# Kernel tuning notes

Hardware: AMD Instinct MI355X
Metric: run time of the kernel (lower is better)

Reference implementation:

```python
import jax, jax.numpy as jnp
import numpy as np
import math

B, S, D_MODEL = 4, 2048, 1024
H, D_HEAD = 16, 64
INIT_RANGE = 0.02


def setup_inputs() -> dict:
    key = jax.random.key(0)
    ks = jax.random.split(key, 10)
    x = jax.random.normal(ks[0], (B, S, D_MODEL), dtype=jnp.float32)
    # torch Linear(in,out): y = x @ W.T + b. We store weights pre-transposed as [H, in, out].
    u = lambda k, shape: jax.random.uniform(k, shape, dtype=jnp.float32, minval=-INIT_RANGE, maxval=INIT_RANGE)
    wq = u(ks[1], (H, D_MODEL, D_HEAD))
    wk = u(ks[2], (H, D_MODEL, D_HEAD))
    wv = u(ks[3], (H, D_MODEL, D_HEAD))
    wo = u(ks[4], (H, D_HEAD, D_MODEL))
    # biases: torch default init is uniform(-1/sqrt(fan_in), 1/sqrt(fan_in)); values don't matter for correctness harness
    bq = u(ks[5], (H, D_HEAD))
    bk = u(ks[6], (H, D_HEAD))
    bv = u(ks[7], (H, D_HEAD))
    bo = u(ks[8], (H, D_MODEL))
    return {"normalized_resid_pre": x, "wq": wq, "bq": bq, "wk": wk, "bk": bk,
            "wv": wv, "bv": bv, "wo": wo, "bo": bo}


def reference(normalized_resid_pre, wq, bq, wk, bk, wv, bv, wo, bo):
    x = normalized_resid_pre  # [B, S, D]
    # Batched multi-head QKV projections (original does a python loop per head)
    q = jnp.einsum('bsd,hde->bhse', x, wq) + bq[None, :, None, :]  # [B,H,S,dh]
    k = jnp.einsum('bsd,hde->bhse', x, wk) + bk[None, :, None, :]
    v = jnp.einsum('bsd,hde->bhse', x, wv) + bv[None, :, None, :]
    scale = 1.0 / math.sqrt(D_HEAD)  # cfg.global_d_head, used unconditionally
    scores = jnp.einsum('bhse,bhte->bhst', q, k) * scale  # [B,H,S,S], non-causal
    attn = jax.nn.softmax(scores, axis=-1)
    heads = jnp.einsum('bhst,bhte->bhse', attn, v)  # [B,H,S,dh]
    # per-head output projections, summed over heads (= sum of per-head Linear outputs)
    out = jnp.einsum('bhse,hed->bsd', heads, wo) + jnp.sum(bo, axis=0)[None, None, :]
    return out
```

## Files before the change

### kernel.cpp

```cpp
#include <hip/hip_runtime.h>
#include <hip/hip_bf16.h>
#include <math.h>


typedef __attribute__((ext_vector_type(8))) short bf16x8;
typedef __attribute__((ext_vector_type(4))) float f32x4;

#define GLDS16(gsrc, lbase) \
    __builtin_amdgcn_global_load_lds((const __attribute__((address_space(1))) void*)(gsrc), \
                                     (__attribute__((address_space(3))) void*)(lbase), 16, 0, 0)

static __device__ __forceinline__ ushort f2bf(float f) {
    __bf16 h = (__bf16)f;
    return *reinterpret_cast<ushort*>(&h);
}
static __device__ __forceinline__ unsigned pk_bf16(float a, float b) {
    return (unsigned)f2bf(a) | ((unsigned)f2bf(b) << 16);
}
static __device__ __forceinline__ float clampf(float v) {
    return fminf(fmaxf(v, -1e30f), 1e30f);
}

__global__ void cvt_x(const float* __restrict__ x, ushort* __restrict__ xb) {
    int idx = blockIdx.x * 256 + threadIdx.x;
    float4 a = ((const float4*)x)[idx * 2];
    float4 b = ((const float4*)x)[idx * 2 + 1];
    uint4 o;
    o.x = pk_bf16(a.x, a.y);
    o.y = pk_bf16(a.z, a.w);
    o.z = pk_bf16(b.x, b.y);
    o.w = pk_bf16(b.z, b.w);
    ((uint4*)xb)[idx] = o;
}

__global__ void pack_wqkv(const float* __restrict__ wq, const float* __restrict__ wk,
                          const float* __restrict__ wv, const float* __restrict__ bq,
                          const float* __restrict__ bk, const float* __restrict__ bv,
                          ushort* __restrict__ WT, float* __restrict__ biasc) {
    __shared__ __align__(16) ushort Lt[64][72];
    int bid = blockIdx.x;
    int kt = bid & 15, h = (bid >> 4) & 15, proj = bid >> 8;
    const float* w  = (proj == 0) ? wq : (proj == 1) ? wk : wv;
    const float* bb = (proj == 0) ? bq : (proj == 1) ? bk : bv;
    int t = threadIdx.x;
    int e = t & 63, kr = t >> 6;
    const float* src = w + (size_t)h * 65536 + (size_t)kt * 64 * 64 + e;
    #pragma unroll
    for (int i = 0; i < 16; ++i) {
        int kl = kr * 16 + i;
        Lt[e][kl] = f2bf(src[(size_t)kl * 64]);
    }
    if (kt == 0 && t < 64) biasc[proj * 1024 + h * 64 + t] = bb[h * 64 + t];
    __syncthreads();
    int eo = t >> 2, kc = (t & 3) * 16;
    size_t dst = (size_t)(proj * 1024 + h * 64 + eo) * 1024 + kt * 64 + kc;
    *(bf16x8*)(WT + dst)     = *(const bf16x8*)(&Lt[eo][kc]);
    *(bf16x8*)(WT + dst + 8) = *(const bf16x8*)(&Lt[eo][kc + 8]);
}
__global__ void pack_wo(const float* __restrict__ wo, const float* __restrict__ bo,
                        ushort* __restrict__ WoT, float* __restrict__ biaso) {
    __shared__ __align__(16) ushort Lt[64][72];
    int bid = blockIdx.x;
    int het = bid & 15, dt = bid >> 4;
    int t = threadIdx.x;
    int dl = t & 63, hw = t >> 6;
    #pragma unroll
    for (int i = 0; i < 16; ++i) {
        int hel = hw * 16 + i;
        Lt[dl][hel] = f2bf(wo[(size_t)(het * 64 + hel) * 1024 + dt * 64 + dl]);
    }
    if (het == 0 && t < 64) {
        int d = dt * 64 + t;
        float s = 0.f;
        for (int hh = 0; hh < 16; ++hh) s += bo[hh * 1024 + d];
        biaso[d] = s;
    }
    __syncthreads();
    int do_ = t >> 2, hc = (t & 3) * 16;
    size_t dst = (size_t)(dt * 64 + do_) * 1024 + het * 64 + hc;
    *(bf16x8*)(WoT + dst)     = *(const bf16x8*)(&Lt[do_][hc]);
    *(bf16x8*)(WoT + dst + 8) = *(const bf16x8*)(&Lt[do_][hc + 8]);
}

__global__ __launch_bounds__(256, 2) void gemm_bt(
    const ushort* __restrict__ A, const ushort* __restrict__ Bt,
    const float* __restrict__ bias, ushort* __restrict__ C, ushort* __restrict__ Vt,
    float* __restrict__ Cf, int M, int N, int K, int ldc, int n_split)
{
    __shared__ __align__(16) ushort Al[128][64];
    __shared__ __align__(16) ushort Bl[128][64];
    const int t = threadIdx.x;
    const int lane = t & 63, wave = t >> 6;
    const int wr = wave >> 1, wc = wave & 1;
    const int quad = lane >> 4, l16 = lane & 15;
    const int row0 = blockIdx.x * 128, col0 = blockIdx.y * 128;
    const int sr = t >> 3;
    const int scx = ((t & 7) ^ (sr & 7)) * 8;
    const int xk = l16 & 7;

    f32x4 acc[4][4] = {};

    for (int kt = 0; kt < K; kt += 64) {
        char* abase = (char*)Al + wave * 1024;
        char* bbase = (char*)Bl + wave * 1024;
        const ushort* ag = A  + (size_t)(row0 + sr) * K + kt + scx;
        const ushort* bg = Bt + (size_t)(col0 + sr) * K + kt + scx;
        #pragma unroll
        for (int i = 0; i < 4; ++i) {
            GLDS16(ag + (size_t)i * 32 * K, abase + i * 4096);
            GLDS16(bg + (size_t)i * 32 * K, bbase + i * 4096);
        }
        __syncthreads();
        #pragma unroll
        for (int ks = 0; ks < 2; ++ks) {
            bf16x8 a[4], b[4];
            #pragma unroll
            for (int mi = 0; mi < 4; ++mi)
                a[mi] = *(const bf16x8*)(&Al[wr * 64 + mi * 16 + l16][((ks * 4 + quad) ^ xk) * 8]);
            #pragma unroll
            for (int ni = 0; ni < 4; ++ni)
                b[ni] = *(const bf16x8*)(&Bl[wc * 64 + ni * 16 + l16][((ks * 4 + quad) ^ xk) * 8]);
            #pragma unroll
            for (int mi = 0; mi < 4; ++mi)
                #pragma unroll
                for (int ni = 0; ni < 4; ++ni)
                    acc[mi][ni] = __builtin_amdgcn_mfma_f32_16x16x32_bf16(a[mi], b[ni], acc[mi][ni], 0, 0, 0);
        }
        __syncthreads();
    }
    #pragma unroll
    for (int mi = 0; mi < 4; ++mi) {
        int rowb = row0 + wr * 64 + mi * 16 + quad * 4;
        #pragma unroll
        for (int ni = 0; ni < 4; ++ni) {
            int col = col0 + wc * 64 + ni * 16 + l16;
            float bs = bias ? bias[col] : 0.f;
            #pragma unroll
            for (int r = 0; r < 4; ++r) {
                float v = clampf(acc[mi][ni][r] + bs);
                int row = rowb + r;
                if (Cf) {
                    Cf[(size_t)row * ldc + col] = v;
                } else if (col < n_split) {
                    C[(size_t)row * ldc + col] = f2bf(v);
                } else {
                    int bb = row >> 11, s = row & 2047;
                    int pos = (s & ~63) | (((s & 15) << 2) | ((s >> 4) & 3));
                    Vt[(size_t)bb * (1024 * 2048) + (size_t)(col - n_split) * 2048 + pos] = f2bf(v);
                }
            }
        }
    }
}

__global__ __launch_bounds__(256, 2) void attn(
    const ushort* __restrict__ QK, const ushort* __restrict__ Vt, ushort* __restrict__ O)
{
    __shared__ __align__(16) ushort Kl[64][64];
    __shared__ __align__(16) ushort Vl[64][64];
    __shared__ __align__(16) ushort Pl[4][32][72];
    const int qt = blockIdx.x, b = blockIdx.y, h = blockIdx.z;
    const int t = threadIdx.x, lane = t & 63, wave = t >> 6;
    const int quad = lane >> 4, l16 = lane & 15;
    const int rowq0 = b * 2048 + qt * 128 + wave * 32;
    const int sr = t >> 3;
    const int scx = ((t & 7) ^ (sr & 7)) * 8;
    const int xk = l16 & 7;
    const float cscale = 0.125f * 1.44269504088896340736f;
    const float M0 = 14.0f;

    bf16x8 qf[2][2];
    #pragma unroll
    for (int mi = 0; mi < 2; ++mi)
        #pragma unroll
        for (int ks = 0; ks < 2; ++ks)
            qf[mi][ks] = *(const bf16x8*)(QK + (size_t)(rowq0 + mi * 16 + l16) * 2048
                                          + h * 64 + ks * 32 + quad * 8);

    f32x4 of[2][4] = {};
    float lpart[2][4] = {};

    for (int kt = 0; kt < 2048; kt += 64) {
        {
            char* kbase = (char*)Kl + wave * 1024;
            char* vbase = (char*)Vl + wave * 1024;
            const ushort* kg = QK + (size_t)(b * 2048 + kt + sr) * 2048 + 1024 + h * 64 + scx;
            const ushort* vg = Vt + (size_t)b * (1024 * 2048) + (size_t)(h * 64 + sr) * 2048 + kt + scx;
            GLDS16(kg, kbase);
            GLDS16(kg + 32 * 2048, kbase + 4096);
            GLDS16(vg, vbase);
            GLDS16(vg + 32 * 2048, vbase + 4096);
        }
        __syncthreads();

        f32x4 sf[2][4] = {};
        #pragma unroll
        for (int ks = 0; ks < 2; ++ks) {
            bf16x8 kb[4];
            #pragma unroll
            for (int nt = 0; nt < 4; ++nt)
                kb[nt] = *(const bf16x8*)(&Kl[nt * 16 + l16][((ks * 4 + quad) ^ xk) * 8]);
            #pragma unroll
            for (int mi = 0; mi < 2; ++mi)
                #pragma unroll
                for (int nt = 0; nt < 4; ++nt)
                    sf[mi][nt] = __builtin_amdgcn_mfma_f32_16x16x32_bf16(qf[mi][ks], kb[nt], sf[mi][nt], 0, 0, 0);
        }

        #pragma unroll
        for (int mi = 0; mi < 2; ++mi) {
            #pragma unroll
            for (int r = 0; r < 4; ++r) {
                float p0 = exp2f(sf[mi][0][r] * cscale - M0);
                float p1 = exp2f(sf[mi][1][r] * cscale - M0);
                float p2 = exp2f(sf[mi][2][r] * cscale - M0);
                float p3 = exp2f(sf[mi][3][r] * cscale - M0);
                lpart[mi][r] += (p0 + p1) + (p2 + p3);
                int prw = mi * 16 + quad * 4 + r;
                uint2 pk;
                pk.x = pk_bf16(p0, p1);
                pk.y = pk_bf16(p2, p3);
                *(uint2*)(&Pl[wave][prw][l16 * 4]) = pk;
            }
        }

        #pragma unroll
        for (int ks = 0; ks < 2; ++ks) {
            bf16x8 pa[2];
            #pragma unroll
            for (int mi = 0; mi < 2; ++mi)
                pa[mi] = *(const bf16x8*)(&Pl[wave][mi * 16 + l16][ks * 32 + quad * 8]);
            #pragma unroll
            for (int nt = 0; nt < 4; ++nt) {
                bf16x8 vb = *(const bf16x8*)(&Vl[nt * 16 + l16][((ks * 4 + quad) ^ xk) * 8]);
                #pragma unroll
                for (int mi = 0; mi < 2; ++mi)
                    of[mi][nt] = __builtin_amdgcn_mfma_f32_16x16x32_bf16(pa[mi], vb, of[mi][nt], 0, 0, 0);
            }
        }
        __syncthreads();
    }

    #pragma unroll
    for (int mi = 0; mi < 2; ++mi) {
        #pragma unroll
        for (int r = 0; r < 4; ++r) {
            float l = lpart[mi][r];
            #pragma unroll
            for (int d = 1; d < 16; d <<= 1) l += __shfl_xor(l, d, 64);
            float inv = 1.0f / fmaxf(l, 1e-30f);
            int row = rowq0 + mi * 16 + quad * 4 + r;
            #pragma unroll
            for (int nt = 0; nt < 4; ++nt)
                O[(size_t)row * 1024 + h * 64 + nt * 16 + l16] = f2bf(clampf(of[mi][nt][r] * inv));
        }
    }
}

extern "C" void kernel_launch(void* const* d_in, const int* in_sizes, int n_in,
                              void* d_out, int out_size, void* d_ws, size_t ws_size,
                              hipStream_t stream) {
    const float* x  = (const float*)d_in[0];
    const float* wq = (const float*)d_in[1];
    const float* bq = (const float*)d_in[2];
    const float* wk = (const float*)d_in[3];
    const float* bk = (const float*)d_in[4];
    const float* wv = (const float*)d_in[5];
    const float* bv = (const float*)d_in[6];
    const float* wo = (const float*)d_in[7];
    const float* bo = (const float*)d_in[8];

    char* ws = (char*)d_ws;
    const size_t MB = 1024 * 1024;
    ushort* xb    = (ushort*)(ws);
    ushort* WqkvT = (ushort*)(ws + 16 * MB);
    ushort* WoT   = (ushort*)(ws + 22 * MB);
    float*  biasc = (float*) (ws + 24 * MB);
    float*  biaso = (float*) (ws + 24 * MB + 64 * 1024);
    ushort* C1    = (ushort*)(ws + 25 * MB);
    ushort* Vt    = (ushort*)(ws + 57 * MB);
    ushort* Obuf  = (ushort*)(ws + 73 * MB);

    cvt_x    <<<4096, 256, 0, stream>>>(x, xb);
    pack_wqkv<<<768, 256, 0, stream>>>(wq, wk, wv, bq, bk, bv, WqkvT, biasc);
    pack_wo  <<<256, 256, 0, stream>>>(wo, bo, WoT, biaso);

    gemm_bt<<<dim3(64, 24), 256, 0, stream>>>(xb, WqkvT, biasc, C1, Vt, nullptr,
                                              8192, 3072, 1024, 2048, 2048);
    attn<<<dim3(16, 4, 16), 256, 0, stream>>>(C1, Vt, Obuf);
    gemm_bt<<<dim3(64, 8), 256, 0, stream>>>(Obuf, WoT, biaso, nullptr, nullptr, (float*)d_out,
                                             8192, 1024, 1024, 1024, 0);
}
```

Baseline: 343.6 us.

## Double-buffer K/V tiles in attention and move V transpose to separate kernel

The attention kernel now double-buffers its K and V shared-memory tiles. The next tile's global-to-LDS loads are issued before computing on the current one, which drops one barrier per iteration and overlaps memory latency with MFMA work. The QKV GEMM epilogue no longer scatters V into the transposed layout with strided stores. It writes a contiguous 3072-wide output, and a new transpose_v kernel builds Vt through LDS with coalesced 16-byte stores. This costs an extra launch plus an extra read and write of V, and doubles the LDS used by the K/V tiles.

```diff
diff --git a/kernel.cpp b/kernel.cpp
--- a/kernel.cpp
+++ b/kernel.cpp
@@ -82,10 +82,31 @@
     *(bf16x8*)(WoT + dst + 8) = *(const bf16x8*)(&Lt[do_][hc + 8]);
 }
 
+__global__ void transpose_v(const ushort* __restrict__ C1x, ushort* __restrict__ Vt) {
+    __shared__ ushort Lt[64][72];
+    int st = blockIdx.x, b = blockIdx.y, h = blockIdx.z;
+    int t = threadIdx.x;
+    int r = t >> 3, c = (t & 7) * 8;
+    #pragma unroll
+    for (int i = 0; i < 2; ++i) {
+        int sl = r + i * 32;
+        bf16x8 v = *(const bf16x8*)(C1x + (size_t)(b * 2048 + st * 64 + sl) * 3072
+                                    + 2048 + h * 64 + c);
+        int pos = ((sl & 15) << 2) | (sl >> 4);
+        #pragma unroll
+        for (int j = 0; j < 8; ++j) Lt[c + j][pos] = (ushort)v[j];
+    }
+    __syncthreads();
+    int e = t >> 2, ch = (t & 3) * 16;
+    size_t dst = (size_t)b * (1024 * 2048) + (size_t)(h * 64 + e) * 2048 + st * 64 + ch;
+    *(bf16x8*)(Vt + dst)     = *(const bf16x8*)(&Lt[e][ch]);
+    *(bf16x8*)(Vt + dst + 8) = *(const bf16x8*)(&Lt[e][ch + 8]);
+}
+
 __global__ __launch_bounds__(256, 2) void gemm_bt(
     const ushort* __restrict__ A, const ushort* __restrict__ Bt,
-    const float* __restrict__ bias, ushort* __restrict__ C, ushort* __restrict__ Vt,
-    float* __restrict__ Cf, int M, int N, int K, int ldc, int n_split)
+    const float* __restrict__ bias, ushort* __restrict__ C,
+    float* __restrict__ Cf, int M, int N, int K, int ldc)
 {
     __shared__ __align__(16) ushort Al[128][64];
     __shared__ __align__(16) ushort Bl[128][64];
@@ -139,15 +160,8 @@
             for (int r = 0; r < 4; ++r) {
                 float v = clampf(acc[mi][ni][r] + bs);
                 int row = rowb + r;
-                if (Cf) {
-                    Cf[(size_t)row * ldc + col] = v;
-                } else if (col < n_split) {
-                    C[(size_t)row * ldc + col] = f2bf(v);
-                } else {
-                    int bb = row >> 11, s = row & 2047;
-                    int pos = (s & ~63) | (((s & 15) << 2) | ((s >> 4) & 3));
-                    Vt[(size_t)bb * (1024 * 2048) + (size_t)(col - n_split) * 2048 + pos] = f2bf(v);
-                }
+                if (Cf) Cf[(size_t)row * ldc + col] = v;
+                else    C [(size_t)row * ldc + col] = f2bf(v);
             }
         }
     }
@@ -156,8 +170,8 @@
 __global__ __launch_bounds__(256, 2) void attn(
     const ushort* __restrict__ QK, const ushort* __restrict__ Vt, ushort* __restrict__ O)
 {
-    __shared__ __align__(16) ushort Kl[64][64];
-    __shared__ __align__(16) ushort Vl[64][64];
+    __shared__ __align__(16) ushort Kl[2][64][64];
+    __shared__ __align__(16) ushort Vl[2][64][64];
     __shared__ __align__(16) ushort Pl[4][32][72];
     const int qt = blockIdx.x, b = blockIdx.y, h = blockIdx.z;
     const int t = threadIdx.x, lane = t & 63, wave = t >> 6;
@@ -169,29 +183,44 @@
     const float cscale = 0.125f * 1.44269504088896340736f;
     const float M0 = 14.0f;
 
+    const ushort* kg0 = QK + (size_t)(b * 2048 + sr) * 3072 + 1024 + h * 64 + scx;
+    const ushort* vg0 = Vt + (size_t)b * (1024 * 2048) + (size_t)(h * 64 + sr) * 2048 + scx;
+
+    {
+        char* kbase = (char*)Kl[0] + wave * 1024;
+        char* vbase = (char*)Vl[0] + wave * 1024;
+        GLDS16(kg0, kbase);
+        GLDS16(kg0 + (size_t)32 * 3072, kbase + 4096);
+        GLDS16(vg0, vbase);
+        GLDS16(vg0 + 32 * 2048, vbase + 4096);
+    }
+
     bf16x8 qf[2][2];
     #pragma unroll
     for (int mi = 0; mi < 2; ++mi)
         #pragma unroll
         for (int ks = 0; ks < 2; ++ks)
-            qf[mi][ks] = *(const bf16x8*)(QK + (size_t)(rowq0 + mi * 16 + l16) * 2048
+            qf[mi][ks] = *(const bf16x8*)(QK + (size_t)(rowq0 + mi * 16 + l16) * 3072
                                           + h * 64 + ks * 32 + quad * 8);
 
     f32x4 of[2][4] = {};
     float lpart[2][4] = {};
 
-    for (int kt = 0; kt < 2048; kt += 64) {
-        {
-            char* kbase = (char*)Kl + wave * 1024;
-            char* vbase = (char*)Vl + wave * 1024;
-            const ushort* kg = QK + (size_t)(b * 2048 + kt + sr) * 2048 + 1024 + h * 64 + scx;
-            const ushort* vg = Vt + (size_t)b * (1024 * 2048) + (size_t)(h * 64 + sr) * 2048 + kt + scx;
+    __syncthreads();
+
+    for (int i = 0; i < 32; ++i) {
+        const int buf = i & 1;
+        if (i < 31) {
+            int kn = (i + 1) * 64;
+            char* kbase = (char*)Kl[buf ^ 1] + wave * 1024;
+            char* vbase = (char*)Vl[buf ^ 1] + wave * 1024;
+            const ushort* kg = kg0 + (size_t)kn * 3072;
+            const ushort* vg = vg0 + kn;
             GLDS16(kg, kbase);
-            GLDS16(kg + 32 * 2048, kbase + 4096);
+            GLDS16(kg + (size_t)32 * 3072, kbase + 4096);
             GLDS16(vg, vbase);
             GLDS16(vg + 32 * 2048, vbase + 4096);
         }
-        __syncthreads();
 
         f32x4 sf[2][4] = {};
         #pragma unroll
@@ -199,7 +228,7 @@
             bf16x8 kb[4];
             #pragma unroll
             for (int nt = 0; nt < 4; ++nt)
-                kb[nt] = *(const bf16x8*)(&Kl[nt * 16 + l16][((ks * 4 + quad) ^ xk) * 8]);
+                kb[nt] = *(const bf16x8*)(&Kl[buf][nt * 16 + l16][((ks * 4 + quad) ^ xk) * 8]);
             #pragma unroll
             for (int mi = 0; mi < 2; ++mi)
                 #pragma unroll
@@ -232,7 +261,7 @@
                 pa[mi] = *(const bf16x8*)(&Pl[wave][mi * 16 + l16][ks * 32 + quad * 8]);
             #pragma unroll
             for (int nt = 0; nt < 4; ++nt) {
-                bf16x8 vb = *(const bf16x8*)(&Vl[nt * 16 + l16][((ks * 4 + quad) ^ xk) * 8]);
+                bf16x8 vb = *(const bf16x8*)(&Vl[buf][nt * 16 + l16][((ks * 4 + quad) ^ xk) * 8]);
                 #pragma unroll
                 for (int mi = 0; mi < 2; ++mi)
                     of[mi][nt] = __builtin_amdgcn_mfma_f32_16x16x32_bf16(pa[mi], vb, of[mi][nt], 0, 0, 0);
@@ -277,17 +306,18 @@
     ushort* WoT   = (ushort*)(ws + 22 * MB);
     float*  biasc = (float*) (ws + 24 * MB);
     float*  biaso = (float*) (ws + 24 * MB + 64 * 1024);
-    ushort* C1    = (ushort*)(ws + 25 * MB);
-    ushort* Vt    = (ushort*)(ws + 57 * MB);
-    ushort* Obuf  = (ushort*)(ws + 73 * MB);
+    ushort* C1x   = (ushort*)(ws + 25 * MB);
+    ushort* Vt    = (ushort*)(ws + 73 * MB);
+    ushort* Obuf  = xb;
 
     cvt_x    <<<4096, 256, 0, stream>>>(x, xb);
     pack_wqkv<<<768, 256, 0, stream>>>(wq, wk, wv, bq, bk, bv, WqkvT, biasc);
     pack_wo  <<<256, 256, 0, stream>>>(wo, bo, WoT, biaso);
 
-    gemm_bt<<<dim3(64, 24), 256, 0, stream>>>(xb, WqkvT, biasc, C1, Vt, nullptr,
-                                              8192, 3072, 1024, 2048, 2048);
-    attn<<<dim3(16, 4, 16), 256, 0, stream>>>(C1, Vt, Obuf);
-    gemm_bt<<<dim3(64, 8), 256, 0, stream>>>(Obuf, WoT, biaso, nullptr, nullptr, (float*)d_out,
-                                             8192, 1024, 1024, 1024, 0);
-}
+    gemm_bt<<<dim3(64, 24), 256, 0, stream>>>(xb, WqkvT, biasc, C1x, nullptr,
+                                              8192, 3072, 1024, 3072);
+    transpose_v<<<dim3(32, 4, 16), 256, 0, stream>>>(C1x, Vt);
+    attn<<<dim3(16, 4, 16), 256, 0, stream>>>(C1x, Vt, Obuf);
+    gemm_bt<<<dim3(64, 8), 256, 0, stream>>>(Obuf, WoT, biaso, nullptr, (float*)d_out,
+                                             8192, 1024, 1024, 1024);
+}
```

Measured after the change: 336.5 us. 1.02x faster.
